# Kernel tuning notes

Hardware: AMD Instinct MI355X
Metric: run time of the kernel (lower is better)

The kernel has to match this reference:

```python
import jax, jax.numpy as jnp
import numpy as np
import math

D_MODEL = 1024
NUM_HEADS = 16
MAX_LEN = 2048
D_HEAD = D_MODEL // NUM_HEADS
BATCH = 2
SEQ = 2048


def setup_inputs() -> dict:
    root = jax.random.key(0)
    ks = jax.random.split(root, 10)
    s = 1.0 / math.sqrt(D_MODEL)
    return {
        "query": jax.random.normal(ks[0], (BATCH, SEQ, D_MODEL), jnp.float32),
        "key": jax.random.normal(ks[1], (BATCH, SEQ, D_MODEL), jnp.float32),
        "value": jax.random.normal(ks[2], (BATCH, SEQ, D_MODEL), jnp.float32),
        "Wq": jax.random.normal(ks[3], (D_MODEL, D_MODEL), jnp.float32) * s,
        "bq": jax.random.normal(ks[4], (D_MODEL,), jnp.float32) * s,
        "Wk": jax.random.normal(ks[5], (D_MODEL, D_MODEL), jnp.float32) * s,
        "bk": jax.random.normal(ks[6], (D_MODEL,), jnp.float32) * s,
        "Wv": jax.random.normal(ks[7], (D_MODEL, D_MODEL), jnp.float32) * s,
        "bv": jax.random.normal(ks[8], (D_MODEL,), jnp.float32) * s,
        "Er": jax.random.normal(ks[9], (MAX_LEN, D_HEAD), jnp.float32),
    }


def _skew(QEr):
    # QEr: [B, H, S, S] -> pad one zero column on the left, reshape, drop first row
    B, H, R, C = QEr.shape
    padded = jnp.pad(QEr, ((0, 0), (0, 0), (0, 0), (1, 0)))  # [B,H,R,C+1]
    reshaped = padded.reshape(B, H, C + 1, R)
    return reshaped[:, :, 1:, :]  # [B,H,R,C] == Srel


def reference(query, key, value, Wq, bq, Wk, bk, Wv, bv, Er):
    B, S, D = query.shape
    H, dh = NUM_HEADS, D_HEAD
    # nn.Linear: x @ W.T + b
    q = (jnp.einsum("bsd,ed->bse", query, Wq) + bq).reshape(B, S, H, dh).transpose(0, 2, 1, 3)  # [B,H,S,dh]
    k = (jnp.einsum("bsd,ed->bse", key, Wk) + bk).reshape(B, S, H, dh).transpose(0, 2, 1, 3)
    v = (jnp.einsum("bsd,ed->bse", value, Wv) + bv).reshape(B, S, H, dh).transpose(0, 2, 1, 3)
    start = MAX_LEN - S
    Er_s = Er[start:, :]  # [S, dh]
    QEr = jnp.einsum("bhsd,ld->bhsl", q, Er_s)  # [B,H,S,S]
    Srel = _skew(QEr)
    QK = jnp.einsum("bhsd,bhtd->bhst", q, k)
    attn = (QK + Srel) / math.sqrt(dh)
    causal = jnp.tril(jnp.ones((S, S), dtype=bool))
    attn = jnp.where(causal[None, None], attn, -jnp.inf)
    attn = jax.nn.softmax(attn, axis=-1)
    out = jnp.einsum("bhst,bhtd->bhsd", attn, v)  # [B,H,S,dh]
    out = out.transpose(0, 2, 1, 3).reshape(B, S, D)
    return out  # dropout is identity in eval mode
```

## Files before the change

### kernel.cpp

```cpp
#include <hip/hip_runtime.h>
#include <hip/hip_bf16.h>

typedef __attribute__((ext_vector_type(8))) short bf16x8;
typedef __attribute__((ext_vector_type(4))) float f32x4;

#define DEVI __device__ __forceinline__
#define AS1 __attribute__((address_space(1)))
#define AS3 __attribute__((address_space(3)))

constexpr int SEQ_   = 2048;
constexpr int HEADS  = 16;
constexpr int DHEAD  = 64;
constexpr int DMODEL = 1024;

DEVI unsigned short f2bf(float x) {
  __hip_bfloat16 h = __float2bfloat16(x);
  return __builtin_bit_cast(unsigned short, h);
}

DEVI f32x4 MFMA(bf16x8 a, bf16x8 b, f32x4 c) {
  return __builtin_amdgcn_mfma_f32_16x16x32_bf16(a, b, c, 0, 0, 0);
}

__global__ void conv3_kernel(const float* s0, const float* s1, const float* s2,
                             unsigned short* d0, unsigned short* d1, unsigned short* d2,
                             int n) {
  const float* s = (blockIdx.y == 0) ? s0 : (blockIdx.y == 1) ? s1 : s2;
  unsigned short* d = (blockIdx.y == 0) ? d0 : (blockIdx.y == 1) ? d1 : d2;
  int i = (blockIdx.x * 256 + threadIdx.x) * 8;
  if (i >= n) return;
  const float4* p = (const float4*)(s + i);
  float4 v0 = p[0], v1 = p[1];
  union { unsigned short u[8]; bf16x8 v; } t;
  t.u[0] = f2bf(v0.x); t.u[1] = f2bf(v0.y); t.u[2] = f2bf(v0.z); t.u[3] = f2bf(v0.w);
  t.u[4] = f2bf(v1.x); t.u[5] = f2bf(v1.y); t.u[6] = f2bf(v1.z); t.u[7] = f2bf(v1.w);
  *(bf16x8*)(d + i) = t.v;
}

__global__ void conv4_kernel(const float* s0, const float* s1, const float* s2,
                             const float* s3,
                             unsigned short* d0, unsigned short* d1,
                             unsigned short* d2, unsigned short* d3,
                             int n_w, int n_e) {
  const int y = blockIdx.y;
  const float* s = (y == 0) ? s0 : (y == 1) ? s1 : (y == 2) ? s2 : s3;
  unsigned short* d = (y == 0) ? d0 : (y == 1) ? d1 : (y == 2) ? d2 : d3;
  const int n = (y == 3) ? n_e : n_w;
  int i = (blockIdx.x * 256 + threadIdx.x) * 8;
  if (i >= n) return;
  const float4* p = (const float4*)(s + i);
  float4 v0 = p[0], v1 = p[1];
  union { unsigned short u[8]; bf16x8 v; } t;
  t.u[0] = f2bf(v0.x); t.u[1] = f2bf(v0.y); t.u[2] = f2bf(v0.z); t.u[3] = f2bf(v0.w);
  t.u[4] = f2bf(v1.x); t.u[5] = f2bf(v1.y); t.u[6] = f2bf(v1.z); t.u[7] = f2bf(v1.w);
  *(bf16x8*)(d + i) = t.v;
}

__global__ __launch_bounds__(256) void proj3_kernel(
    const unsigned short* __restrict__ X0, const unsigned short* __restrict__ X1,
    const unsigned short* __restrict__ X2,
    const unsigned short* __restrict__ W0, const unsigned short* __restrict__ W1,
    const unsigned short* __restrict__ W2,
    const float* __restrict__ bi0, const float* __restrict__ bi1,
    const float* __restrict__ bi2,
    unsigned short* __restrict__ o0, unsigned short* __restrict__ o1,
    unsigned short* __restrict__ o2) {
  const int z = blockIdx.z;
  const unsigned short* X = (z == 0) ? X0 : (z == 1) ? X1 : X2;
  const unsigned short* W = (z == 0) ? W0 : (z == 1) ? W1 : W2;
  const float* bias        = (z == 0) ? bi0 : (z == 1) ? bi1 : bi2;
  unsigned short* out      = (z == 0) ? o0 : (z == 1) ? o1 : o2;

  __shared__ unsigned short Abuf[2][128 * 32];
  __shared__ unsigned short Bbuf[2][128 * 32];
  const int tid  = threadIdx.x;
  const int lane = tid & 63, wv = tid >> 6;
  const int q = lane >> 4, r = lane & 15;
  const int wrow = wv >> 1, wcol = wv & 1;
  const int rowA0 = blockIdx.x * 128, colB0 = blockIdx.y * 128;

  const char* Ag = (const char*)(X + (size_t)rowA0 * DMODEL);
  const char* Bg = (const char*)(W + (size_t)colB0 * DMODEL);

  f32x4 acc[4][4] = {};

  auto stage = [&](int ks, int buf) {
    const int koff = ks * 64;
#pragma unroll
    for (int i = 0; i < 2; ++i) {
      const int b   = (i * 256 + tid) * 16;
      const int row = b >> 6, col = b & 63;
      __builtin_amdgcn_global_load_lds(
          (const AS1 void*)(Ag + (size_t)row * (DMODEL * 2) + koff + col),
          (AS3 void*)((char*)&Abuf[buf][0] + i * 4096 + wv * 1024),
          16, 0, 0);
      __builtin_amdgcn_global_load_lds(
          (const AS1 void*)(Bg + (size_t)row * (DMODEL * 2) + koff + col),
          (AS3 void*)((char*)&Bbuf[buf][0] + i * 4096 + wv * 1024),
          16, 0, 0);
    }
  };

  stage(0, 0);
  for (int ks = 0; ks < 32; ++ks) {
    __syncthreads();
    if (ks + 1 < 32) stage(ks + 1, (ks + 1) & 1);
    const unsigned short* A  = &Abuf[ks & 1][0];
    const unsigned short* Bt = &Bbuf[ks & 1][0];
    bf16x8 af[4], bfr[4];
#pragma unroll
    for (int t = 0; t < 4; ++t) {
      af[t]  = *(const bf16x8*)(A  + (wrow * 64 + t * 16 + r) * 32 + q * 8);
      bfr[t] = *(const bf16x8*)(Bt + (wcol * 64 + t * 16 + r) * 32 + q * 8);
    }
#pragma unroll
    for (int m = 0; m < 4; ++m)
#pragma unroll
      for (int n = 0; n < 4; ++n)
        acc[m][n] = MFMA(af[m], bfr[n], acc[m][n]);
  }

#pragma unroll
  for (int m = 0; m < 4; ++m) {
#pragma unroll
    for (int n = 0; n < 4; ++n) {
      const int e  = colB0 + wcol * 64 + n * 16 + r;
      const float bv = bias[e];
      const int h = e >> 6, dd = e & 63;
      const int nrow0 = rowA0 + wrow * 64 + m * 16 + q * 4;
      const int bb = nrow0 >> 11, ss0 = nrow0 & 2047;
      const size_t bh = (size_t)(bb * HEADS + h);
      if (z == 0) {
#pragma unroll
        for (int j = 0; j < 4; ++j)
          out[(bh * SEQ_ + (ss0 + j)) * DHEAD + dd] = f2bf((acc[m][n][j] + bv) * 0.125f);
      } else if (z == 1) {
#pragma unroll
        for (int j = 0; j < 4; ++j) {
          const int s = ss0 + j;
          const size_t off = (bh * 64 + (size_t)(s >> 5)) * 2048
                           + (size_t)(((dd >> 5) * 2 + ((s >> 4) & 1)) * 512)
                           + (size_t)(((((dd & 31) >> 3) << 4) + (s & 15)) * 8)
                           + (dd & 7);
          out[off] = f2bf(acc[m][n][j] + bv);
        }
      } else {
        union { unsigned short u[4]; uint2 v; } pk;
#pragma unroll
        for (int j = 0; j < 4; ++j) pk.u[j] = f2bf(acc[m][n][j] + bv);
        const size_t off = (bh * 64 + (size_t)(ss0 >> 5)) * 2048
                         + (size_t)((dd >> 4) * 512)
                         + (size_t)(((((ss0 & 31) >> 3) << 4) + (dd & 15)) * 8)
                         + (ss0 & 7);
        *(uint2*)&out[off] = pk.v;
      }
    }
  }
}

__global__ __launch_bounds__(256, 2) void attn_kernel(
    const unsigned short* __restrict__ qb, const unsigned short* __restrict__ kt,
    const unsigned short* __restrict__ vt, const unsigned short* __restrict__ Er,
    float* __restrict__ out) {
  __shared__ unsigned short k_lds[3][4096];
  __shared__ unsigned short v_lds[3][4096];
  __shared__ unsigned short p_lds[4][32][72];

  const int tid  = threadIdx.x;
  const int lane = tid & 63, wv = tid >> 6;
  const int q = lane >> 4, r = lane & 15;

  const int lid = blockIdx.x;
  const int xcd = lid & 7, idx = lid >> 3;
  const int bh  = (xcd << 2) | (idx & 3);
  const int T   = 15 - (idx >> 2);
  const int s0  = T * 128 + wv * 32;
  const int nIter = 2 * T + 2;
  const int bb = bh >> 4, hh = bh & 15;

  const unsigned short* qbh = qb + (size_t)bh * SEQ_ * DHEAD;
  const char* ktb = (const char*)(kt + (size_t)bh * 64 * 2048);
  const char* vtb = (const char*)(vt + (size_t)bh * 64 * 2048);
  const f32x4 zero4 = {0.f, 0.f, 0.f, 0.f};

  const char* sgbase = (wv < 2) ? ktb : vtb;
  char* sdst0 = (char*)((wv < 2) ? &k_lds[0][0] : &v_lds[0][0]);
  const int shalf = (wv & 1) * 4096;
  const int soff  = lane * 16;

  auto stageKV = [&](int it, int buf) {
    const int g = (it < nIter) ? it : nIter - 1;
    const char* src = sgbase + (size_t)g * 8192 + shalf + soff;
    char* dst = sdst0 + buf * 8192 + shalf;
#pragma unroll
    for (int c = 0; c < 4; ++c)
      __builtin_amdgcn_global_load_lds((const AS1 void*)(src + c * 1024),
                                       (AS3 void*)(dst + c * 1024), 16, 0, 0);
  };

  struct ErSet { bf16x8 e[8]; };
  auto loadE = [&](ErSet& es, int it) {
    const int lb = 2016 + it * 64 - s0;
#pragma unroll
    for (int mi = 0; mi < 4; ++mi) {
      int l = lb + 32 + mi * 16 + r;
      l = l < 2047 ? l : 2047;
      es.e[mi * 2 + 0] = *(const bf16x8*)(Er + (size_t)l * DHEAD + q * 8);
      es.e[mi * 2 + 1] = *(const bf16x8*)(Er + (size_t)l * DHEAD + 32 + q * 8);
    }
  };

  bf16x8 qf[2][2];
#pragma unroll
  for (int rt = 0; rt < 2; ++rt) {
    qf[rt][0] = *(const bf16x8*)(qbh + (size_t)(s0 + rt * 16 + r) * DHEAD + q * 8);
    qf[rt][1] = *(const bf16x8*)(qbh + (size_t)(s0 + rt * 16 + r) * DHEAD + 32 + q * 8);
  }
  stageKV(0, 0);

  f32x4 qer[2][6];
  {
    const int lb = 2016 - s0;
#pragma unroll
    for (int m = 0; m < 2; ++m) {
      const int l = lb + m * 16 + r;
      bf16x8 e0 = *(const bf16x8*)(Er + (size_t)l * DHEAD + q * 8);
      bf16x8 e1 = *(const bf16x8*)(Er + (size_t)l * DHEAD + 32 + q * 8);
#pragma unroll
      for (int rt = 0; rt < 2; ++rt)
        qer[rt][m] = MFMA(qf[rt][1], e1, MFMA(qf[rt][0], e0, zero4));
    }
  }

  f32x4 oacc[2][4] = {};
  float lpart[2][4] = {};

  ErSet eA, eB;
  loadE(eA, 0);

  auto body = [&](int it, int cur, const ErSet& es) {
    const int t0 = it * 64;
    if (t0 > s0 + 31) return;
    const unsigned short* KL = &k_lds[cur][0];
    const unsigned short* VL = &v_lds[cur][0];

    bf16x8 kf[4][2];
#pragma unroll
    for (int ct = 0; ct < 4; ++ct)
#pragma unroll
      for (int kc = 0; kc < 2; ++kc)
        kf[ct][kc] = *(const bf16x8*)(KL + (ct >> 1) * 2048 + (kc * 2 + (ct & 1)) * 512 + lane * 8);

    f32x4 s4[2][4];
    __builtin_amdgcn_s_setprio(1);
#pragma unroll
    for (int rt = 0; rt < 2; ++rt)
#pragma unroll
      for (int ct = 0; ct < 4; ++ct)
        s4[rt][ct] = MFMA(qf[rt][1], kf[ct][1], MFMA(qf[rt][0], kf[ct][0], zero4));
#pragma unroll
    for (int rt = 0; rt < 2; ++rt)
#pragma unroll
      for (int mi = 0; mi < 4; ++mi)
        qer[rt][2 + mi] = MFMA(qf[rt][1], es.e[mi * 2 + 1],
                               MFMA(qf[rt][0], es.e[mi * 2 + 0], zero4));
    __builtin_amdgcn_s_setprio(0);

    const int d0 = t0 - s0;
#pragma unroll
    for (int rt = 0; rt < 2; ++rt) {
#pragma unroll
      for (int j = 0; j < 4; ++j) {
        const int srcl = (q << 4) | ((15 + r - q * 4 - j) & 15);
        float g0 = __shfl(qer[rt][1 - rt][j], srcl);
        float g1 = __shfl(qer[rt][2 - rt][j], srcl);
        float g2 = __shfl(qer[rt][3 - rt][j], srcl);
        float g3 = __shfl(qer[rt][4 - rt][j], srcl);
        float g4 = __shfl(qer[rt][5 - rt][j], srcl);
        const bool hi = (r > q * 4 + j);
        const float b0 = hi ? g1 : g0;
        const float b1 = hi ? g2 : g1;
        const float b2 = hi ? g3 : g2;
        const float b3 = hi ? g4 : g3;
        const int A_ = rt * 16 + q * 4 + j - r - d0;
        const float p0 = (A_ >= 0)  ? __expf(s4[rt][0][j] + b0) : 0.f;
        const float p1 = (A_ >= 16) ? __expf(s4[rt][1][j] + b1) : 0.f;
        const float p2 = (A_ >= 32) ? __expf(s4[rt][2][j] + b2) : 0.f;
        const float p3 = (A_ >= 48) ? __expf(s4[rt][3][j] + b3) : 0.f;
        lpart[rt][j] += (p0 + p1) + (p2 + p3);
        const int sl = rt * 16 + q * 4 + j;
        p_lds[wv][sl][r]      = f2bf(p0);
        p_lds[wv][sl][16 + r] = f2bf(p1);
        p_lds[wv][sl][32 + r] = f2bf(p2);
        p_lds[wv][sl][48 + r] = f2bf(p3);
      }
    }

    bf16x8 vf[4][2];
#pragma unroll
    for (int dc = 0; dc < 4; ++dc)
#pragma unroll
      for (int tc = 0; tc < 2; ++tc)
        vf[dc][tc] = *(const bf16x8*)(VL + tc * 2048 + dc * 512 + lane * 8);
    __builtin_amdgcn_s_setprio(1);
#pragma unroll
    for (int rt = 0; rt < 2; ++rt) {
      bf16x8 pf0 = *(const bf16x8*)(&p_lds[wv][rt * 16 + r][0] + q * 8);
      bf16x8 pf1 = *(const bf16x8*)(&p_lds[wv][rt * 16 + r][0] + 32 + q * 8);
#pragma unroll
      for (int dc = 0; dc < 4; ++dc)
        oacc[rt][dc] = MFMA(pf1, vf[dc][1], MFMA(pf0, vf[dc][0], oacc[rt][dc]));
    }
    __builtin_amdgcn_s_setprio(0);

#pragma unroll
    for (int rt = 0; rt < 2; ++rt) { qer[rt][0] = qer[rt][4]; qer[rt][1] = qer[rt][5]; }
  };

  int it = 0, cur = 0;
  while (true) {
    int nxt = cur + 1; if (nxt == 3) nxt = 0;
    stageKV(it + 1, nxt);
    loadE(eB, it + 1);
    asm volatile("s_waitcnt vmcnt(12)\n\ts_barrier" ::: "memory");
    body(it, cur, eA);
    cur = nxt;
    if (++it >= nIter) break;
    nxt = cur + 1; if (nxt == 3) nxt = 0;
    stageKV(it + 1, nxt);
    loadE(eA, it + 1);
    asm volatile("s_waitcnt vmcnt(12)\n\ts_barrier" ::: "memory");
    body(it, cur, eB);
    cur = nxt;
    if (++it >= nIter) break;
  }

#pragma unroll
  for (int rt = 0; rt < 2; ++rt)
#pragma unroll
    for (int j = 0; j < 4; ++j) {
      float ls = lpart[rt][j];
#pragma unroll
      for (int d = 1; d < 16; d <<= 1) ls += __shfl_xor(ls, d);
      const float inv = 1.0f / ls;
      const int ss = s0 + rt * 16 + q * 4 + j;
#pragma unroll
      for (int dc = 0; dc < 4; ++dc) {
        const int dd = dc * 16 + r;
        out[((size_t)(bb * SEQ_ + ss)) * DMODEL + hh * DHEAD + dd] = oacc[rt][dc][j] * inv;
      }
    }
}

extern "C" void kernel_launch(void* const* d_in, const int* in_sizes, int n_in,
                              void* d_out, int out_size, void* d_ws, size_t ws_size,
                              hipStream_t stream) {
  const float* query = (const float*)d_in[0];
  const float* key   = (const float*)d_in[1];
  const float* value = (const float*)d_in[2];
  const float* Wq    = (const float*)d_in[3];
  const float* bq    = (const float*)d_in[4];
  const float* Wk    = (const float*)d_in[5];
  const float* bk    = (const float*)d_in[6];
  const float* Wv    = (const float*)d_in[7];
  const float* bv    = (const float*)d_in[8];
  const float* Er    = (const float*)d_in[9];

  char* ws = (char*)d_ws;
  unsigned short* qb   = (unsigned short*)(ws + (0u  << 20));
  unsigned short* ktil = (unsigned short*)(ws + (8u  << 20));
  unsigned short* vtil = (unsigned short*)(ws + (16u << 20));
  unsigned short* Xq   = (unsigned short*)(ws + (32u << 20));
  unsigned short* Xk   = (unsigned short*)(ws + (40u << 20));
  unsigned short* Xv   = (unsigned short*)(ws + (48u << 20));
  unsigned short* Wqb  = (unsigned short*)(ws + (56u << 20));
  unsigned short* Wkb  = (unsigned short*)(ws + (58u << 20));
  unsigned short* Wvb  = (unsigned short*)(ws + (60u << 20));
  unsigned short* Erb  = (unsigned short*)(ws + (62u << 20));

  conv3_kernel<<<dim3(2048, 3), 256, 0, stream>>>(query, key, value, Xq, Xk, Xv,
                                                  2 * SEQ_ * DMODEL);
  conv4_kernel<<<dim3(512, 4), 256, 0, stream>>>(Wq, Wk, Wv, Er,
                                                 Wqb, Wkb, Wvb, Erb,
                                                 DMODEL * DMODEL, SEQ_ * DHEAD);

  proj3_kernel<<<dim3(32, 8, 3), 256, 0, stream>>>(Xq, Xk, Xv, Wqb, Wkb, Wvb,
                                                   bq, bk, bv, qb, ktil, vtil);

  attn_kernel<<<dim3(512), 256, 0, stream>>>(qb, ktil, vtil, Erb, (float*)d_out);
}
```

Before: 144.5 us.

## Balance causal attention by splitting key ranges across paired blocks with reduce pass

Each attention block now processes two query strips: a long strip for one tile and part of a complementary strip, so every block does roughly equal causal work instead of blocks for late query tiles doing far more. Partial outputs and row sums from the split strips go to workspace, and a new reduce kernel combines them and normalizes. The V tile layout is changed to a 64-key permuted layout, and the bias shuffles and P writes pack two floats into bf16 pairs to cut shuffle and LDS store count. This costs an extra kernel launch, extra global traffic for partials, and a reused workspace region that overlaps the Xk/Xv buffers.

```diff
diff --git a/kernel.cpp b/kernel.cpp
--- a/kernel.cpp
+++ b/kernel.cpp
@@ -20,6 +20,12 @@
 
 DEVI f32x4 MFMA(bf16x8 a, bf16x8 b, f32x4 c) {
   return __builtin_amdgcn_mfma_f32_16x16x32_bf16(a, b, c, 0, 0, 0);
+}
+
+DEVI unsigned int cvtpk(float lo, float hi) {
+  unsigned int u;
+  asm("v_cvt_pk_bf16_f32 %0, %1, %2" : "=v"(u) : "v"(lo), "v"(hi));
+  return u;
 }
 
 __global__ void conv3_kernel(const float* s0, const float* s1, const float* s2,
@@ -145,26 +151,31 @@
           out[off] = f2bf(acc[m][n][j] + bv);
         }
       } else {
-        union { unsigned short u[4]; uint2 v; } pk;
-#pragma unroll
-        for (int j = 0; j < 4; ++j) pk.u[j] = f2bf(acc[m][n][j] + bv);
-        const size_t off = (bh * 64 + (size_t)(ss0 >> 5)) * 2048
-                         + (size_t)((dd >> 4) * 512)
-                         + (size_t)(((((ss0 & 31) >> 3) << 4) + (dd & 15)) * 8)
-                         + (ss0 & 7);
-        *(uint2*)&out[off] = pk.v;
+#pragma unroll
+        for (int j = 0; j < 4; ++j) {
+          const int s = ss0 + j;
+          const int tile64 = s >> 6, t = s & 63;
+          const int tp = 4 * (t & 15) + (t >> 4);
+          const int tc = tp >> 5, u = tp & 31;
+          const int ln = ((u >> 3) << 4) | (dd & 15);
+          const size_t off = (bh * 32 + (size_t)tile64) * 4096
+                           + (size_t)(tc * 2048 + (dd >> 4) * 512 + ln * 8 + (u & 7));
+          out[off] = f2bf(acc[m][n][j] + bv);
+        }
       }
     }
   }
 }
+
+struct ErSet { bf16x8 e[8]; };
 
 __global__ __launch_bounds__(256, 2) void attn_kernel(
     const unsigned short* __restrict__ qb, const unsigned short* __restrict__ kt,
     const unsigned short* __restrict__ vt, const unsigned short* __restrict__ Er,
-    float* __restrict__ out) {
+    float* __restrict__ out, float* __restrict__ pO1, float* __restrict__ pL) {
   __shared__ unsigned short k_lds[3][4096];
   __shared__ unsigned short v_lds[3][4096];
-  __shared__ unsigned short p_lds[4][32][72];
+  __shared__ unsigned short p_lds[4][32][68];
 
   const int tid  = threadIdx.x;
   const int lane = tid & 63, wv = tid >> 6;
@@ -173,14 +184,13 @@
   const int lid = blockIdx.x;
   const int xcd = lid & 7, idx = lid >> 3;
   const int bh  = (xcd << 2) | (idx & 3);
-  const int T   = 15 - (idx >> 2);
-  const int s0  = T * 128 + wv * 32;
-  const int nIter = 2 * T + 2;
+  const int jb  = idx >> 2;
+  const int p = jb >> 1, role = jb & 1;
   const int bb = bh >> 4, hh = bh & 15;
 
   const unsigned short* qbh = qb + (size_t)bh * SEQ_ * DHEAD;
   const char* ktb = (const char*)(kt + (size_t)bh * 64 * 2048);
-  const char* vtb = (const char*)(vt + (size_t)bh * 64 * 2048);
+  const char* vtb = (const char*)(vt + (size_t)bh * 32 * 4096);
   const f32x4 zero4 = {0.f, 0.f, 0.f, 0.f};
 
   const char* sgbase = (wv < 2) ? ktb : vtb;
@@ -189,8 +199,7 @@
   const int soff  = lane * 16;
 
   auto stageKV = [&](int it, int buf) {
-    const int g = (it < nIter) ? it : nIter - 1;
-    const char* src = sgbase + (size_t)g * 8192 + shalf + soff;
+    const char* src = sgbase + (size_t)it * 8192 + shalf + soff;
     char* dst = sdst0 + buf * 8192 + shalf;
 #pragma unroll
     for (int c = 0; c < 4; ++c)
@@ -198,158 +207,210 @@
                                        (AS3 void*)(dst + c * 1024), 16, 0, 0);
   };
 
-  struct ErSet { bf16x8 e[8]; };
-  auto loadE = [&](ErSet& es, int it) {
-    const int lb = 2016 + it * 64 - s0;
-#pragma unroll
-    for (int mi = 0; mi < 4; ++mi) {
-      int l = lb + 32 + mi * 16 + r;
-      l = l < 2047 ? l : 2047;
-      es.e[mi * 2 + 0] = *(const bf16x8*)(Er + (size_t)l * DHEAD + q * 8);
-      es.e[mi * 2 + 1] = *(const bf16x8*)(Er + (size_t)l * DHEAD + 32 + q * 8);
-    }
+  auto run_strip = [&](int T, int it0, int it1, float* po, float* pl) {
+    const int s0 = T * 128 + wv * 32;
+    __syncthreads();
+    stageKV(it0, 0);
+
+    bf16x8 qf[2][2];
+#pragma unroll
+    for (int rt = 0; rt < 2; ++rt) {
+      qf[rt][0] = *(const bf16x8*)(qbh + (size_t)(s0 + rt * 16 + r) * DHEAD + q * 8);
+      qf[rt][1] = *(const bf16x8*)(qbh + (size_t)(s0 + rt * 16 + r) * DHEAD + 32 + q * 8);
+    }
+
+    f32x4 qer[2][6];
+    {
+      const int lb0 = 2016 + it0 * 64 - s0;
+#pragma unroll
+      for (int m = 0; m < 2; ++m) {
+        int l = lb0 + m * 16 + r; l = l < 2047 ? l : 2047;
+        bf16x8 e0 = *(const bf16x8*)(Er + (size_t)l * DHEAD + q * 8);
+        bf16x8 e1 = *(const bf16x8*)(Er + (size_t)l * DHEAD + 32 + q * 8);
+#pragma unroll
+        for (int rt = 0; rt < 2; ++rt)
+          qer[rt][m] = MFMA(qf[rt][1], e1, MFMA(qf[rt][0], e0, zero4));
+      }
+    }
+
+    auto loadE = [&](ErSet& es, int it) {
+      const int lb = 2016 + it * 64 - s0;
+#pragma unroll
+      for (int mi = 0; mi < 4; ++mi) {
+        int l = lb + 32 + mi * 16 + r;
+        l = l < 2047 ? l : 2047;
+        es.e[mi * 2 + 0] = *(const bf16x8*)(Er + (size_t)l * DHEAD + q * 8);
+        es.e[mi * 2 + 1] = *(const bf16x8*)(Er + (size_t)l * DHEAD + 32 + q * 8);
+      }
+    };
+
+    f32x4 oacc[2][4] = {};
+    float lpart[2][4] = {};
+
+    auto body = [&](int it, int cur, const ErSet& es) {
+      const int t0 = it * 64;
+      if (t0 > s0 + 31) return;
+      const unsigned short* KL = &k_lds[cur][0];
+      const unsigned short* VL = &v_lds[cur][0];
+
+      bf16x8 kf[4][2];
+#pragma unroll
+      for (int ct = 0; ct < 4; ++ct)
+#pragma unroll
+        for (int kc = 0; kc < 2; ++kc)
+          kf[ct][kc] = *(const bf16x8*)(KL + (ct >> 1) * 2048 + (kc * 2 + (ct & 1)) * 512 + lane * 8);
+
+      f32x4 s4[2][4];
+      __builtin_amdgcn_s_setprio(1);
+#pragma unroll
+      for (int rt = 0; rt < 2; ++rt)
+#pragma unroll
+        for (int ct = 0; ct < 4; ++ct)
+          s4[rt][ct] = MFMA(qf[rt][1], kf[ct][1], MFMA(qf[rt][0], kf[ct][0], zero4));
+#pragma unroll
+      for (int rt = 0; rt < 2; ++rt)
+#pragma unroll
+        for (int mi = 0; mi < 4; ++mi)
+          qer[rt][2 + mi] = MFMA(qf[rt][1], es.e[mi * 2 + 1],
+                                 MFMA(qf[rt][0], es.e[mi * 2 + 0], zero4));
+      __builtin_amdgcn_s_setprio(0);
+
+      const int d0 = t0 - s0;
+#pragma unroll
+      for (int rt = 0; rt < 2; ++rt) {
+        const int a = 1 - rt;
+#pragma unroll
+        for (int j = 0; j < 4; ++j) {
+          unsigned int pkA = cvtpk(qer[rt][a][j],     qer[rt][a + 1][j]);
+          unsigned int pkB = cvtpk(qer[rt][a + 2][j], qer[rt][a + 3][j]);
+          const float  s5f = qer[rt][a + 4][j];
+          const int srcl = (q << 4) | ((15 + r - q * 4 - j) & 15);
+          unsigned int A = (unsigned int)__shfl((int)pkA, srcl);
+          unsigned int B = (unsigned int)__shfl((int)pkB, srcl);
+          const float g4 = __shfl(s5f, srcl);
+          const float g0 = __builtin_bit_cast(float, A << 16);
+          const float g1 = __builtin_bit_cast(float, A & 0xffff0000u);
+          const float g2 = __builtin_bit_cast(float, B << 16);
+          const float g3 = __builtin_bit_cast(float, B & 0xffff0000u);
+          const bool hi = (r > q * 4 + j);
+          const float b0 = hi ? g1 : g0;
+          const float b1 = hi ? g2 : g1;
+          const float b2 = hi ? g3 : g2;
+          const float b3 = hi ? g4 : g3;
+          const int A_ = rt * 16 + q * 4 + j - r - d0;
+          const float p0 = (A_ >= 0)  ? __expf(s4[rt][0][j] + b0) : 0.f;
+          const float p1 = (A_ >= 16) ? __expf(s4[rt][1][j] + b1) : 0.f;
+          const float p2 = (A_ >= 32) ? __expf(s4[rt][2][j] + b2) : 0.f;
+          const float p3 = (A_ >= 48) ? __expf(s4[rt][3][j] + b3) : 0.f;
+          lpart[rt][j] += (p0 + p1) + (p2 + p3);
+          const int sl = rt * 16 + q * 4 + j;
+          const unsigned long long pw =
+              (unsigned long long)cvtpk(p0, p1) |
+              ((unsigned long long)cvtpk(p2, p3) << 32);
+          *(unsigned long long*)&p_lds[wv][sl][4 * r] = pw;
+        }
+      }
+
+      bf16x8 vf[4][2];
+#pragma unroll
+      for (int dc = 0; dc < 4; ++dc)
+#pragma unroll
+        for (int tc = 0; tc < 2; ++tc)
+          vf[dc][tc] = *(const bf16x8*)(VL + tc * 2048 + dc * 512 + lane * 8);
+      __builtin_amdgcn_s_setprio(1);
+#pragma unroll
+      for (int rt = 0; rt < 2; ++rt) {
+        bf16x8 pf0 = *(const bf16x8*)(&p_lds[wv][rt * 16 + r][0] + q * 8);
+        bf16x8 pf1 = *(const bf16x8*)(&p_lds[wv][rt * 16 + r][0] + 32 + q * 8);
+#pragma unroll
+        for (int dc = 0; dc < 4; ++dc)
+          oacc[rt][dc] = MFMA(pf1, vf[dc][1], MFMA(pf0, vf[dc][0], oacc[rt][dc]));
+      }
+      __builtin_amdgcn_s_setprio(0);
+
+#pragma unroll
+      for (int rt = 0; rt < 2; ++rt) { qer[rt][0] = qer[rt][4]; qer[rt][1] = qer[rt][5]; }
+    };
+
+    ErSet eA, eB;
+    loadE(eA, it0);
+
+    int it = it0, cur = 0;
+    while (true) {
+      int nx = cur + 1; if (nx == 3) nx = 0;
+      int itn = (it + 1 < it1) ? it + 1 : it1 - 1;
+      stageKV(itn, nx);
+      loadE(eB, itn);
+      asm volatile("s_waitcnt vmcnt(12)\n\ts_barrier" ::: "memory");
+      body(it, cur, eA);
+      cur = nx;
+      if (++it >= it1) break;
+      nx = cur + 1; if (nx == 3) nx = 0;
+      itn = (it + 1 < it1) ? it + 1 : it1 - 1;
+      stageKV(itn, nx);
+      loadE(eA, itn);
+      asm volatile("s_waitcnt vmcnt(12)\n\ts_barrier" ::: "memory");
+      body(it, cur, eB);
+      cur = nx;
+      if (++it >= it1) break;
+    }
+
+#pragma unroll
+    for (int rt = 0; rt < 2; ++rt)
+#pragma unroll
+      for (int j = 0; j < 4; ++j) {
+        float ls = lpart[rt][j];
+#pragma unroll
+        for (int d = 1; d < 16; d <<= 1) ls += __shfl_xor(ls, d);
+        const int row = wv * 32 + rt * 16 + q * 4 + j;
+        if (po) {
+#pragma unroll
+          for (int dc = 0; dc < 4; ++dc)
+            po[(size_t)row * 64 + dc * 16 + r] = oacc[rt][dc][j];
+        } else {
+          const int ss = T * 128 + row;
+#pragma unroll
+          for (int dc = 0; dc < 4; ++dc)
+            out[((size_t)(bb * SEQ_ + ss)) * DMODEL + hh * DHEAD + dc * 16 + r] = oacc[rt][dc][j];
+        }
+        if (r == 0) pl[row] = ls;
+      }
   };
 
-  bf16x8 qf[2][2];
-#pragma unroll
-  for (int rt = 0; rt < 2; ++rt) {
-    qf[rt][0] = *(const bf16x8*)(qbh + (size_t)(s0 + rt * 16 + r) * DHEAD + q * 8);
-    qf[rt][1] = *(const bf16x8*)(qbh + (size_t)(s0 + rt * 16 + r) * DHEAD + 32 + q * 8);
+  int TA, a1, TB, b0, b1;
+  if (role == 0) { TA = 15 - p; a1 = 16 - p; TB = p;      b0 = p + 1;  b1 = 2 * p + 2; }
+  else           { TA = p;      a1 = p + 1;  TB = 15 - p; b0 = 16 - p; b1 = 32 - 2 * p; }
+
+  run_strip(TA, 0, a1, nullptr,
+            pL + ((size_t)(bh * 16 + TA)) * 256);
+  run_strip(TB, b0, b1, pO1 + ((size_t)(bh * 16 + TB)) * 8192,
+            pL + ((size_t)(bh * 16 + TB)) * 256 + 128);
+}
+
+__global__ __launch_bounds__(256) void reduce_kernel(const float* __restrict__ pO1,
+                                                     const float* __restrict__ pL,
+                                                     float* __restrict__ out) {
+  const int slot = blockIdx.x;
+  const int bh = slot >> 4, T = slot & 15;
+  const int bb = bh >> 4, hh = bh & 15;
+  const int tid = threadIdx.x;
+  const int row = tid >> 1, half = (tid & 1) * 32;
+
+  const float l0 = pL[(size_t)slot * 256 + row];
+  const float l1 = pL[(size_t)slot * 256 + 128 + row];
+  const float inv = 1.0f / (l0 + l1);
+
+  float* a = out + ((size_t)(bb * SEQ_) + T * 128 + row) * DMODEL + hh * DHEAD + half;
+  const float* b = pO1 + (size_t)slot * 8192 + row * 64 + half;
+#pragma unroll
+  for (int k = 0; k < 8; ++k) {
+    float4 x = ((const float4*)a)[k];
+    float4 y = ((const float4*)b)[k];
+    float4 o;
+    o.x = (x.x + y.x) * inv; o.y = (x.y + y.y) * inv;
+    o.z = (x.z + y.z) * inv; o.w = (x.w + y.w) * inv;
+    ((float4*)a)[k] = o;
   }
-  stageKV(0, 0);
-
-  f32x4 qer[2][6];
-  {
-    const int lb = 2016 - s0;
-#pragma unroll
-    for (int m = 0; m < 2; ++m) {
-      const int l = lb + m * 16 + r;
-      bf16x8 e0 = *(const bf16x8*)(Er + (size_t)l * DHEAD + q * 8);
-      bf16x8 e1 = *(const bf16x8*)(Er + (size_t)l * DHEAD + 32 + q * 8);
-#pragma unroll
-      for (int rt = 0; rt < 2; ++rt)
-        qer[rt][m] = MFMA(qf[rt][1], e1, MFMA(qf[rt][0], e0, zero4));
-    }
-  }
-
-  f32x4 oacc[2][4] = {};
-  float lpart[2][4] = {};
-
-  ErSet eA, eB;
-  loadE(eA, 0);
-
-  auto body = [&](int it, int cur, const ErSet& es) {
-    const int t0 = it * 64;
-    if (t0 > s0 + 31) return;
-    const unsigned short* KL = &k_lds[cur][0];
-    const unsigned short* VL = &v_lds[cur][0];
-
-    bf16x8 kf[4][2];
-#pragma unroll
-    for (int ct = 0; ct < 4; ++ct)
-#pragma unroll
-      for (int kc = 0; kc < 2; ++kc)
-        kf[ct][kc] = *(const bf16x8*)(KL + (ct >> 1) * 2048 + (kc * 2 + (ct & 1)) * 512 + lane * 8);
-
-    f32x4 s4[2][4];
-    __builtin_amdgcn_s_setprio(1);
-#pragma unroll
-    for (int rt = 0; rt < 2; ++rt)
-#pragma unroll
-      for (int ct = 0; ct < 4; ++ct)
-        s4[rt][ct] = MFMA(qf[rt][1], kf[ct][1], MFMA(qf[rt][0], kf[ct][0], zero4));
-#pragma unroll
-    for (int rt = 0; rt < 2; ++rt)
-#pragma unroll
-      for (int mi = 0; mi < 4; ++mi)
-        qer[rt][2 + mi] = MFMA(qf[rt][1], es.e[mi * 2 + 1],
-                               MFMA(qf[rt][0], es.e[mi * 2 + 0], zero4));
-    __builtin_amdgcn_s_setprio(0);
-
-    const int d0 = t0 - s0;
-#pragma unroll
-    for (int rt = 0; rt < 2; ++rt) {
-#pragma unroll
-      for (int j = 0; j < 4; ++j) {
-        const int srcl = (q << 4) | ((15 + r - q * 4 - j) & 15);
-        float g0 = __shfl(qer[rt][1 - rt][j], srcl);
-        float g1 = __shfl(qer[rt][2 - rt][j], srcl);
-        float g2 = __shfl(qer[rt][3 - rt][j], srcl);
-        float g3 = __shfl(qer[rt][4 - rt][j], srcl);
-        float g4 = __shfl(qer[rt][5 - rt][j], srcl);
-        const bool hi = (r > q * 4 + j);
-        const float b0 = hi ? g1 : g0;
-        const float b1 = hi ? g2 : g1;
-        const float b2 = hi ? g3 : g2;
-        const float b3 = hi ? g4 : g3;
-        const int A_ = rt * 16 + q * 4 + j - r - d0;
-        const float p0 = (A_ >= 0)  ? __expf(s4[rt][0][j] + b0) : 0.f;
-        const float p1 = (A_ >= 16) ? __expf(s4[rt][1][j] + b1) : 0.f;
-        const float p2 = (A_ >= 32) ? __expf(s4[rt][2][j] + b2) : 0.f;
-        const float p3 = (A_ >= 48) ? __expf(s4[rt][3][j] + b3) : 0.f;
-        lpart[rt][j] += (p0 + p1) + (p2 + p3);
-        const int sl = rt * 16 + q * 4 + j;
-        p_lds[wv][sl][r]      = f2bf(p0);
-        p_lds[wv][sl][16 + r] = f2bf(p1);
-        p_lds[wv][sl][32 + r] = f2bf(p2);
-        p_lds[wv][sl][48 + r] = f2bf(p3);
-      }
-    }
-
-    bf16x8 vf[4][2];
-#pragma unroll
-    for (int dc = 0; dc < 4; ++dc)
-#pragma unroll
-      for (int tc = 0; tc < 2; ++tc)
-        vf[dc][tc] = *(const bf16x8*)(VL + tc * 2048 + dc * 512 + lane * 8);
-    __builtin_amdgcn_s_setprio(1);
-#pragma unroll
-    for (int rt = 0; rt < 2; ++rt) {
-      bf16x8 pf0 = *(const bf16x8*)(&p_lds[wv][rt * 16 + r][0] + q * 8);
-      bf16x8 pf1 = *(const bf16x8*)(&p_lds[wv][rt * 16 + r][0] + 32 + q * 8);
-#pragma unroll
-      for (int dc = 0; dc < 4; ++dc)
-        oacc[rt][dc] = MFMA(pf1, vf[dc][1], MFMA(pf0, vf[dc][0], oacc[rt][dc]));
-    }
-    __builtin_amdgcn_s_setprio(0);
-
-#pragma unroll
-    for (int rt = 0; rt < 2; ++rt) { qer[rt][0] = qer[rt][4]; qer[rt][1] = qer[rt][5]; }
-  };
-
-  int it = 0, cur = 0;
-  while (true) {
-    int nxt = cur + 1; if (nxt == 3) nxt = 0;
-    stageKV(it + 1, nxt);
-    loadE(eB, it + 1);
-    asm volatile("s_waitcnt vmcnt(12)\n\ts_barrier" ::: "memory");
-    body(it, cur, eA);
-    cur = nxt;
-    if (++it >= nIter) break;
-    nxt = cur + 1; if (nxt == 3) nxt = 0;
-    stageKV(it + 1, nxt);
-    loadE(eA, it + 1);
-    asm volatile("s_waitcnt vmcnt(12)\n\ts_barrier" ::: "memory");
-    body(it, cur, eB);
-    cur = nxt;
-    if (++it >= nIter) break;
-  }
-
-#pragma unroll
-  for (int rt = 0; rt < 2; ++rt)
-#pragma unroll
-    for (int j = 0; j < 4; ++j) {
-      float ls = lpart[rt][j];
-#pragma unroll
-      for (int d = 1; d < 16; d <<= 1) ls += __shfl_xor(ls, d);
-      const float inv = 1.0f / ls;
-      const int ss = s0 + rt * 16 + q * 4 + j;
-#pragma unroll
-      for (int dc = 0; dc < 4; ++dc) {
-        const int dd = dc * 16 + r;
-        out[((size_t)(bb * SEQ_ + ss)) * DMODEL + hh * DHEAD + dd] = oacc[rt][dc][j] * inv;
-      }
-    }
 }
 
 extern "C" void kernel_launch(void* const* d_in, const int* in_sizes, int n_in,
@@ -370,6 +431,8 @@
   unsigned short* qb   = (unsigned short*)(ws + (0u  << 20));
   unsigned short* ktil = (unsigned short*)(ws + (8u  << 20));
   unsigned short* vtil = (unsigned short*)(ws + (16u << 20));
+  float*          pO1  = (float*)(ws + (24u << 20));
+  float*          pL   = (float*)(ws + (40u << 20));
   unsigned short* Xq   = (unsigned short*)(ws + (32u << 20));
   unsigned short* Xk   = (unsigned short*)(ws + (40u << 20));
   unsigned short* Xv   = (unsigned short*)(ws + (48u << 20));
@@ -387,5 +450,8 @@
   proj3_kernel<<<dim3(32, 8, 3), 256, 0, stream>>>(Xq, Xk, Xv, Wqb, Wkb, Wvb,
                                                    bq, bk, bv, qb, ktil, vtil);
 
-  attn_kernel<<<dim3(512), 256, 0, stream>>>(qb, ktil, vtil, Erb, (float*)d_out);
-}
+  attn_kernel<<<dim3(512), 256, 0, stream>>>(qb, ktil, vtil, Erb,
+                                             (float*)d_out, pO1, pL);
+
+  reduce_kernel<<<dim3(512), 256, 0, stream>>>(pO1, pL, (float*)d_out);
+}
```

New measurement: 141.3 us. -2.2%, faster.
